# Performance work log

Measured on AMD Instinct MI355X. Metric: run time of the kernel, lower is better.

## Reference

```python
import jax, jax.numpy as jnp
import numpy as np

B, N, D_MODEL, LAP = 64, 64, 256, 16


def setup_inputs() -> dict:
    key = jax.random.key(0)
    ks = jax.random.split(key, 8)
    adj = jax.random.randint(ks[0], (B, N, N), 0, 2, dtype=jnp.int32)
    node_feats = jax.random.normal(ks[1], (B, N, D_MODEL), dtype=jnp.float32)
    eigvec = jax.random.normal(ks[2], (B, N, LAP), dtype=jnp.float32)
    W_lap = jax.random.normal(ks[3], (LAP, D_MODEL), dtype=jnp.float32) / np.sqrt(LAP)
    W_edge = jax.random.normal(ks[4], (1 + 2 * LAP, D_MODEL), dtype=jnp.float32) / np.sqrt(1 + 2 * LAP)
    b_edge = jax.random.normal(ks[5], (D_MODEL,), dtype=jnp.float32) * 0.02
    type_embed = jax.random.normal(ks[6], (2, D_MODEL), dtype=jnp.float32)
    graph_tok = jax.random.normal(ks[7], (1, 1, D_MODEL), dtype=jnp.float32)
    return {"adj": adj, "node_feats": node_feats, "eigvec": eigvec,
            "W_lap": W_lap, "W_edge": W_edge, "b_edge": b_edge,
            "type_embed": type_embed, "graph_tok": graph_tok}


def reference(adj, node_feats, eigvec, W_lap, W_edge, b_edge, type_embed, graph_tok):
    b, n, _ = adj.shape
    d = graph_tok.shape[-1]
    # node tokens: feats + LapPE projection
    node_tok = node_feats + jnp.einsum('bnl,ld->bnd', eigvec, W_lap)
    # upper-triangular candidate edges (fixed M = n(n-1)/2, jit-friendly)
    iu, ju = jnp.triu_indices(n, k=1)               # [M]
    valid = adj[:, iu, ju] > 0                       # [B, M]
    # stable compaction: valid edges first (matches torch per-graph extraction order)
    order = jnp.argsort(~valid, axis=1, stable=True) # [B, M]
    src = iu[order]                                  # [B, M]
    dst = ju[order]
    valid_sorted = jnp.take_along_axis(valid, order, axis=1)
    Pu = jnp.take_along_axis(eigvec, src[..., None], axis=1)  # [B, M, LAP]
    Pv = jnp.take_along_axis(eigvec, dst[..., None], axis=1)
    m = src.shape[1]
    edge_in = jnp.concatenate([jnp.ones((b, m, 1), eigvec.dtype), Pu, Pv], axis=-1)
    etok = jnp.einsum('bmf,fd->bmd', edge_in, W_edge) + b_edge + type_embed[1]
    etok = jnp.where(valid_sorted[..., None], etok, 0.0)      # zeros at padding
    pad_mask_edges = ~valid_sorted                             # True = padding
    gtok = jnp.broadcast_to(graph_tok, (b, 1, d))
    seq_embeds = jnp.concatenate([gtok, node_tok, etok], axis=1)  # [B, 1+n+M, d]
    pad_mask = jnp.concatenate([jnp.zeros((b, 1 + n), bool), pad_mask_edges], axis=1)
    return seq_embeds, pad_mask
```

## Files before the change

kernel.cpp:

```cpp
#include <hip/hip_runtime.h>

#define B_ 64
#define N_ 64
#define D_ 256
#define LAP_ 16
#define M_ 2016
#define TOK_ 2081
#define MPB_ 504
#define MPW_ 126

typedef float v4f __attribute__((ext_vector_type(4)));

__device__ __forceinline__ void ij_from_m(int m, int& i, int& j) {
    float fm = (float)m;
    int gi = (int)((127.0f - sqrtf(127.0f * 127.0f - 8.0f * fm)) * 0.5f);
    if (gi < 0) gi = 0;
    if (gi > 62) gi = 62;
    while (gi > 0 && (127 * gi - gi * gi) / 2 > m) gi--;
    while (gi < 62 && (127 * (gi + 1) - (gi + 1) * (gi + 1)) / 2 <= m) gi++;
    i = gi;
    j = gi + 1 + (m - (127 * gi - gi * gi) / 2);
}

__global__ __launch_bounds__(256, 1) void fused_kernel(
    const int*   __restrict__ adj,
    const float* __restrict__ node_feats,
    const float* __restrict__ eigvec,
    const float* __restrict__ W_lap,
    const float* __restrict__ W_edge,
    const float* __restrict__ b_edge,
    const float* __restrict__ type_embed,
    const float* __restrict__ graph_tok,
    float*       __restrict__ out)
{
    __shared__ float sEig[N_ * LAP_];
    __shared__ float sU[N_ * D_];
    __shared__ float sV[N_ * D_];
    __shared__ unsigned long long sWords[32];
    __shared__ int sPref[32];
    __shared__ int sDest[MPB_];
    __shared__ int sTotal;

    const int b    = blockIdx.x;
    const int cg   = blockIdx.y;
    const int t    = threadIdx.x;
    const int wave = t >> 6, lane = t & 63;

    ((float4*)sEig)[t] = ((const float4*)(eigvec + (size_t)b * N_ * LAP_))[t];
#pragma unroll
    for (int k = 0; k < 8; k++) {
        int m = k * 256 + t;
        int valid = 0;
        if (m < M_) {
            int i, j;
            ij_from_m(m, i, j);
            valid = (adj[b * (N_ * N_) + i * N_ + j] > 0) ? 1 : 0;
        }
        unsigned long long blt = __ballot(valid);
        if (lane == 0) sWords[k * 4 + wave] = blt;
    }

    float w1c[LAP_], w2c[LAP_], wlc[LAP_];
#pragma unroll
    for (int l = 0; l < LAP_; l++) {
        w1c[l] = W_edge[(1 + l) * D_ + t];
        w2c[l] = W_edge[(1 + LAP_ + l) * D_ + t];
        wlc[l] = W_lap[l * D_ + t];
    }
    v4f base4 = *((const v4f*)W_edge + lane);
    base4 += *((const v4f*)b_edge + lane);
    base4 += *((const v4f*)(type_embed + D_) + lane);

    __syncthreads();

    if (t < 32) {
        int cnt = __popcll(sWords[t]);
        int inc = cnt;
#pragma unroll
        for (int off = 1; off < 32; off <<= 1) {
            int v = __shfl_up(inc, off);
            if (lane >= off) inc += v;
        }
        sPref[t] = inc - cnt;
        if (t == 31) sTotal = inc;
    }

#pragma unroll 4
    for (int n = 0; n < N_; n++) {
        const v4f* e4 = (const v4f*)(sEig + n * LAP_);
        v4f e0 = e4[0], e1 = e4[1], e2 = e4[2], e3 = e4[3];
        float aU, aV;
        aU  = e0.x * w1c[0]  + e0.y * w1c[1]  + e0.z * w1c[2]  + e0.w * w1c[3];
        aU += e1.x * w1c[4]  + e1.y * w1c[5]  + e1.z * w1c[6]  + e1.w * w1c[7];
        aU += e2.x * w1c[8]  + e2.y * w1c[9]  + e2.z * w1c[10] + e2.w * w1c[11];
        aU += e3.x * w1c[12] + e3.y * w1c[13] + e3.z * w1c[14] + e3.w * w1c[15];
        aV  = e0.x * w2c[0]  + e0.y * w2c[1]  + e0.z * w2c[2]  + e0.w * w2c[3];
        aV += e1.x * w2c[4]  + e1.y * w2c[5]  + e1.z * w2c[6]  + e1.w * w2c[7];
        aV += e2.x * w2c[8]  + e2.y * w2c[9]  + e2.z * w2c[10] + e2.w * w2c[11];
        aV += e3.x * w2c[12] + e3.y * w2c[13] + e3.z * w2c[14] + e3.w * w2c[15];
        sU[n * D_ + t] = aU;
        sV[n * D_ + t] = aV;
    }
    __syncthreads();

    const int total = sTotal;
    float* maskb = out + (size_t)B_ * TOK_ * D_ + (size_t)b * TOK_;
    for (int idx = t; idx < MPB_; idx += 256) {
        int m = cg * MPB_ + idx;
        int w = m >> 6, r = m & 63;
        unsigned long long word = sWords[w];
        int rank = sPref[w] + __popcll(word & ((1ull << r) - 1ull));
        int valid = (int)((word >> r) & 1ull);
        int p = valid ? rank : total + (m - rank);
        int i, j;
        ij_from_m(m, i, j);
        sDest[idx] = i | (j << 6) | (valid << 12) | (p << 13);
        maskb[1 + N_ + p] = valid ? 0.0f : 1.0f;
    }

    float* outB = out + (size_t)b * TOK_ * D_;
#pragma unroll 4
    for (int k = 0; k < 16; k++) {
        int n = cg * 16 + k;
        float a = node_feats[((size_t)b * N_ + n) * D_ + t];
        const float* e = sEig + n * LAP_;
#pragma unroll
        for (int l = 0; l < LAP_; l++) a += e[l] * wlc[l];
        __builtin_nontemporal_store(a, outB + (size_t)(1 + n) * D_ + t);
    }
    if (cg == 0) {
        outB[t] = graph_tok[t];
        if (t < 1 + N_) maskb[t] = 0.0f;
    }
    __syncthreads();

    float* outE = outB + (size_t)(1 + N_) * D_;
#pragma unroll 2
    for (int q = 0; q < MPW_; q++) {
        int info = sDest[wave * MPW_ + q];
        int p = info >> 13;
        v4f val = {0.0f, 0.0f, 0.0f, 0.0f};
        if (info & (1 << 12)) {
            int si = info & 63, di = (info >> 6) & 63;
            v4f u = ((const v4f*)(sU + si * D_))[lane];
            v4f v = ((const v4f*)(sV + di * D_))[lane];
            val = base4 + u + v;
        }
        __builtin_nontemporal_store(val, (v4f*)(outE + (size_t)p * D_) + lane);
    }
}

extern "C" void kernel_launch(void* const* d_in, const int* in_sizes, int n_in,
                              void* d_out, int out_size, void* d_ws, size_t ws_size,
                              hipStream_t stream) {
    const int*   adj        = (const int*)d_in[0];
    const float* node_feats = (const float*)d_in[1];
    const float* eigvec     = (const float*)d_in[2];
    const float* W_lap      = (const float*)d_in[3];
    const float* W_edge     = (const float*)d_in[4];
    const float* b_edge     = (const float*)d_in[5];
    const float* type_embed = (const float*)d_in[6];
    const float* graph_tok  = (const float*)d_in[7];
    float* out = (float*)d_out;

    fused_kernel<<<dim3(B_, 4), dim3(256), 0, stream>>>(
        adj, node_feats, eigvec, W_lap, W_edge, b_edge, type_embed, graph_tok, out);
}
```

Baseline: 179.5 us.

## Split fused kernel into prep and edge-scatter kernels via global workspace

Splits the single fused kernel into a prep kernel and a separate edge kernel. The prep kernel computes the per-node U/V projections, with each block now computing only its own column slice instead of the full table redundantly, and writes them to global workspace along with the edge destination codes. The edge kernel launches 2048 blocks with an XCD-aware batch mapping to scatter the edge tokens with much higher parallelism and occupancy. The aim is to remove the redundant full U/V recomputation and low-occupancy, shared-memory-heavy blocks. The cost is an extra launch and a round trip of U/V through global memory or L2.

Result: no change. 180.5 us (+0.6%).

```diff
diff --git a/kernel.cpp b/kernel.cpp
--- a/kernel.cpp
+++ b/kernel.cpp
@@ -6,8 +6,6 @@
 #define LAP_ 16
 #define M_ 2016
 #define TOK_ 2081
-#define MPB_ 504
-#define MPW_ 126
 
 typedef float v4f __attribute__((ext_vector_type(4)));
 
@@ -22,7 +20,7 @@
     j = gi + 1 + (m - (127 * gi - gi * gi) / 2);
 }
 
-__global__ __launch_bounds__(256, 1) void fused_kernel(
+__global__ __launch_bounds__(256, 4) void prep_kernel(
     const int*   __restrict__ adj,
     const float* __restrict__ node_feats,
     const float* __restrict__ eigvec,
@@ -31,14 +29,13 @@
     const float* __restrict__ b_edge,
     const float* __restrict__ type_embed,
     const float* __restrict__ graph_tok,
-    float*       __restrict__ out)
+    float*       __restrict__ out,
+    float*       __restrict__ wsf,
+    int*         __restrict__ dest)
 {
     __shared__ float sEig[N_ * LAP_];
-    __shared__ float sU[N_ * D_];
-    __shared__ float sV[N_ * D_];
     __shared__ unsigned long long sWords[32];
     __shared__ int sPref[32];
-    __shared__ int sDest[MPB_];
     __shared__ int sTotal;
 
     const int b    = blockIdx.x;
@@ -47,6 +44,7 @@
     const int wave = t >> 6, lane = t & 63;
 
     ((float4*)sEig)[t] = ((const float4*)(eigvec + (size_t)b * N_ * LAP_))[t];
+
 #pragma unroll
     for (int k = 0; k < 8; k++) {
         int m = k * 256 + t;
@@ -60,17 +58,14 @@
         if (lane == 0) sWords[k * 4 + wave] = blt;
     }
 
+    const int colS = cg * 64 + lane;
     float w1c[LAP_], w2c[LAP_], wlc[LAP_];
 #pragma unroll
     for (int l = 0; l < LAP_; l++) {
-        w1c[l] = W_edge[(1 + l) * D_ + t];
-        w2c[l] = W_edge[(1 + LAP_ + l) * D_ + t];
+        w1c[l] = W_edge[(1 + l) * D_ + colS];
+        w2c[l] = W_edge[(1 + LAP_ + l) * D_ + colS];
         wlc[l] = W_lap[l * D_ + t];
     }
-    v4f base4 = *((const v4f*)W_edge + lane);
-    base4 += *((const v4f*)b_edge + lane);
-    base4 += *((const v4f*)(type_embed + D_) + lane);
-
     __syncthreads();
 
     if (t < 32) {
@@ -84,38 +79,23 @@
         sPref[t] = inc - cnt;
         if (t == 31) sTotal = inc;
     }
-
-#pragma unroll 4
-    for (int n = 0; n < N_; n++) {
-        const v4f* e4 = (const v4f*)(sEig + n * LAP_);
-        v4f e0 = e4[0], e1 = e4[1], e2 = e4[2], e3 = e4[3];
-        float aU, aV;
-        aU  = e0.x * w1c[0]  + e0.y * w1c[1]  + e0.z * w1c[2]  + e0.w * w1c[3];
-        aU += e1.x * w1c[4]  + e1.y * w1c[5]  + e1.z * w1c[6]  + e1.w * w1c[7];
-        aU += e2.x * w1c[8]  + e2.y * w1c[9]  + e2.z * w1c[10] + e2.w * w1c[11];
-        aU += e3.x * w1c[12] + e3.y * w1c[13] + e3.z * w1c[14] + e3.w * w1c[15];
-        aV  = e0.x * w2c[0]  + e0.y * w2c[1]  + e0.z * w2c[2]  + e0.w * w2c[3];
-        aV += e1.x * w2c[4]  + e1.y * w2c[5]  + e1.z * w2c[6]  + e1.w * w2c[7];
-        aV += e2.x * w2c[8]  + e2.y * w2c[9]  + e2.z * w2c[10] + e2.w * w2c[11];
-        aV += e3.x * w2c[12] + e3.y * w2c[13] + e3.z * w2c[14] + e3.w * w2c[15];
-        sU[n * D_ + t] = aU;
-        sV[n * D_ + t] = aV;
-    }
     __syncthreads();
 
-    const int total = sTotal;
-    float* maskb = out + (size_t)B_ * TOK_ * D_ + (size_t)b * TOK_;
-    for (int idx = t; idx < MPB_; idx += 256) {
-        int m = cg * MPB_ + idx;
-        int w = m >> 6, r = m & 63;
-        unsigned long long word = sWords[w];
-        int rank = sPref[w] + __popcll(word & ((1ull << r) - 1ull));
-        int valid = (int)((word >> r) & 1ull);
-        int p = valid ? rank : total + (m - rank);
-        int i, j;
-        ij_from_m(m, i, j);
-        sDest[idx] = i | (j << 6) | (valid << 12) | (p << 13);
-        maskb[1 + N_ + p] = valid ? 0.0f : 1.0f;
+    float* Ub = wsf + 256 + (size_t)b * N_ * D_;
+    float* Vb = Ub + (size_t)B_ * N_ * D_;
+#pragma unroll 2
+    for (int n16 = 0; n16 < 16; n16++) {
+        int n = wave * 16 + n16;
+        const float* e = sEig + n * LAP_;
+        float aU = 0.0f, aV = 0.0f;
+#pragma unroll
+        for (int l = 0; l < LAP_; l++) {
+            float el = e[l];
+            aU += el * w1c[l];
+            aV += el * w2c[l];
+        }
+        Ub[n * D_ + colS] = aU;
+        Vb[n * D_ + colS] = aV;
     }
 
     float* outB = out + (size_t)b * TOK_ * D_;
@@ -128,22 +108,56 @@
         for (int l = 0; l < LAP_; l++) a += e[l] * wlc[l];
         __builtin_nontemporal_store(a, outB + (size_t)(1 + n) * D_ + t);
     }
+
+    const int total = sTotal;
+    float* maskb = out + (size_t)B_ * TOK_ * D_ + (size_t)b * TOK_;
+    for (int idx = t; idx < 504; idx += 256) {
+        int m = cg * 504 + idx;
+        int w = m >> 6, r = m & 63;
+        unsigned long long word = sWords[w];
+        int rank = sPref[w] + __popcll(word & ((1ull << r) - 1ull));
+        int valid = (int)((word >> r) & 1ull);
+        int p = valid ? rank : total + (m - rank);
+        int i, j;
+        ij_from_m(m, i, j);
+        dest[b * M_ + m] = i | (j << 6) | (valid << 12) | (p << 13);
+        maskb[1 + N_ + p] = valid ? 0.0f : 1.0f;
+    }
+
     if (cg == 0) {
+        wsf[t] = W_edge[t] + b_edge[t] + type_embed[D_ + t];
         outB[t] = graph_tok[t];
         if (t < 1 + N_) maskb[t] = 0.0f;
     }
-    __syncthreads();
+}
 
-    float* outE = outB + (size_t)(1 + N_) * D_;
-#pragma unroll 2
-    for (int q = 0; q < MPW_; q++) {
-        int info = sDest[wave * MPW_ + q];
+__global__ __launch_bounds__(256, 8) void edge_kernel(
+    const float* __restrict__ wsf,
+    const int*   __restrict__ dest,
+    float*       __restrict__ out)
+{
+    const int bid  = blockIdx.x;
+    const int xcd  = bid & 7;
+    const int idx  = bid >> 3;
+    const int b    = ((idx & 7) << 3) | xcd;
+    const int s    = idx >> 3;
+    const int wave = threadIdx.x >> 6, lane = threadIdx.x & 63;
+
+    v4f base4 = ((const v4f*)wsf)[lane];
+    const float* Ub = wsf + 256 + (size_t)b * N_ * D_;
+    const float* Vb = Ub + (size_t)B_ * N_ * D_;
+    const int* db = dest + b * M_;
+    float* outE = out + (size_t)b * TOK_ * D_ + (size_t)(1 + N_) * D_;
+
+    const int m0 = s * 63;
+    for (int q = m0 + wave; q < m0 + 63; q += 4) {
+        int info = db[q];
         int p = info >> 13;
         v4f val = {0.0f, 0.0f, 0.0f, 0.0f};
         if (info & (1 << 12)) {
             int si = info & 63, di = (info >> 6) & 63;
-            v4f u = ((const v4f*)(sU + si * D_))[lane];
-            v4f v = ((const v4f*)(sV + di * D_))[lane];
+            v4f u = ((const v4f*)(Ub + si * D_))[lane];
+            v4f v = ((const v4f*)(Vb + di * D_))[lane];
             val = base4 + u + v;
         }
         __builtin_nontemporal_store(val, (v4f*)(outE + (size_t)p * D_) + lane);
@@ -163,6 +177,11 @@
     const float* graph_tok  = (const float*)d_in[7];
     float* out = (float*)d_out;
 
-    fused_kernel<<<dim3(B_, 4), dim3(256), 0, stream>>>(
-        adj, node_feats, eigvec, W_lap, W_edge, b_edge, type_embed, graph_tok, out);
+    float* wsf = (float*)d_ws;
+    int*   dest = (int*)(wsf + 256 + 2 * (size_t)B_ * N_ * D_);
+
+    prep_kernel<<<dim3(B_, 4), dim3(256), 0, stream>>>(
+        adj, node_feats, eigvec, W_lap, W_edge, b_edge, type_embed, graph_tok,
+        out, wsf, dest);
+    edge_kernel<<<dim3(2048), dim3(256), 0, stream>>>(wsf, dest, out);
 }
```
